# Optimization experiments

Hardware: AMD Instinct MI355X
Metric: run time of the kernel (lower is better)

## Reference

```python
import jax, jax.numpy as jnp
import numpy as np
from jax import lax

DIM = 512
HEADS = 8
SR = 2  # kernel_and_stride for the KV downsampling conv


def setup_inputs() -> dict:
    key = jax.random.key(0)
    k0, k1, k2, k3 = jax.random.split(key, 4)
    B, C, H, W = 4, DIM, 64, 64
    x = jax.random.normal(k0, (B, C, H, W), dtype=jnp.float32)
    # Conv weights in OIHW layout (matching torch)
    wq = jax.random.normal(k1, (C, C, 1, 1), dtype=jnp.float32) / np.sqrt(C)
    wkv = jax.random.normal(k2, (2 * C, C, SR, SR), dtype=jnp.float32) / np.sqrt(C * SR * SR)
    wout = jax.random.normal(k3, (C, C, 1, 1), dtype=jnp.float32) / np.sqrt(C)
    return {"x": x, "wq": wq, "wkv": wkv, "wout": wout}


def _attend(x, wq, wkv, wout):
    B, C, H, W = x.shape
    d = C // HEADS
    scale = d ** -0.5
    # to_q: 1x1 conv == channel matmul
    q = jnp.einsum('bchw,oc->bohw', x, wq[:, :, 0, 0])
    # to_kv: strided conv, downsamples spatial grid by SR
    kv = lax.conv_general_dilated(
        x, wkv, window_strides=(SR, SR), padding='VALID',
        dimension_numbers=('NCHW', 'OIHW', 'NCHW'))
    k, v = jnp.split(kv, 2, axis=1)  # each [B, C, H/SR, W/SR]

    def to_bhl(t):  # [B, (h d), X, Y] -> [B, h, X*Y, d]
        b, c, xh, xw = t.shape
        return t.reshape(b, HEADS, d, xh * xw).transpose(0, 1, 3, 2)

    qh, kh, vh = to_bhl(q), to_bhl(k), to_bhl(v)
    sim = jnp.einsum('bhid,bhjd->bhij', qh, kh) * scale
    attn = jax.nn.softmax(sim, axis=-1)
    out = jnp.einsum('bhij,bhjd->bhid', attn, vh)  # [B, h, HW, d]
    out = out.transpose(0, 1, 3, 2).reshape(B, C, H, W)
    return jnp.einsum('bchw,oc->bohw', out, wout[:, :, 0, 0])


def reference(x, wq, wkv, wout):
    return _attend(x, wq, wkv, wout)
```

## Files before the change

kernel.cpp:

```cpp
#include <hip/hip_runtime.h>
#include <hip/hip_bf16.h>

typedef __bf16 bf16x8 __attribute__((ext_vector_type(8)));
typedef float f32x4 __attribute__((ext_vector_type(4)));
typedef unsigned short ushort_t;
typedef ushort_t ushort8 __attribute__((ext_vector_type(8)));
typedef unsigned uint2v __attribute__((ext_vector_type(2)));
typedef unsigned uint4v __attribute__((ext_vector_type(4)));

#define DIM 512
#define HEADS 8
#define HD 64
#define HWN 4096
#define KVN 1024
#define KKV 2048
#define LOG2E 1.44269504f

__device__ __forceinline__ ushort_t f2bf(float f) {
    union { float f; unsigned u; } v; v.f = f;
    unsigned r = v.u + 0x7fffu + ((v.u >> 16) & 1u);
    return (ushort_t)(r >> 16);
}

__device__ __forceinline__ unsigned cvtpk(float lo, float hi) {
    unsigned r;
    asm("v_cvt_pk_bf16_f32 %0, %1, %2" : "=v"(r) : "v"(lo), "v"(hi));
    return r;
}

__device__ __forceinline__ void pl32swap(unsigned &a, unsigned &b) {
    asm("v_permlane32_swap_b32 %0, %1" : "+v"(a), "+v"(b));
}
__device__ __forceinline__ void pl16swap(unsigned &a, unsigned &b) {
    asm("v_permlane16_swap_b32 %0, %1" : "+v"(a), "+v"(b));
}

__device__ __forceinline__ bf16x8 frag4(unsigned a, unsigned b, unsigned c, unsigned d) {
    uint4v t; t[0] = a; t[1] = b; t[2] = c; t[3] = d;
    return __builtin_bit_cast(bf16x8, t);
}

__device__ __forceinline__ void gload_lds16(const ushort_t* g, ushort_t* l) {
    __builtin_amdgcn_global_load_lds(
        (const __attribute__((address_space(1))) unsigned int*)(const void*)g,
        (__attribute__((address_space(3))) unsigned int*)(void*)l,
        16, 0, 0);
}

__device__ __forceinline__ void kstep_mfma(
        const ushort_t* __restrict__ ldsA, const ushort_t* __restrict__ ldsB,
        int wm, int wn, int l15, int quad, f32x4 (&acc)[4][4]) {
    bf16x8 a[4], bb[4];
    #pragma unroll
    for (int i = 0; i < 4; ++i)
        a[i] = *(const bf16x8*)&ldsA[(wm + i * 16 + l15) * 32 + quad * 8];
    #pragma unroll
    for (int j = 0; j < 4; ++j)
        bb[j] = *(const bf16x8*)&ldsB[(wn + j * 16 + l15) * 32 + quad * 8];
    #pragma unroll
    for (int i = 0; i < 4; ++i)
        #pragma unroll
        for (int j = 0; j < 4; ++j)
            acc[i][j] = __builtin_amdgcn_mfma_f32_16x16x32_bf16(a[i], bb[j], acc[i][j], 0, 0, 0);
}

__global__ __launch_bounds__(256) void cvt_kernel(
        const float* __restrict__ src, ushort_t* __restrict__ dst, int n8) {
    int i = blockIdx.x * 256 + threadIdx.x;
    if (i >= n8) return;
    const float* p = &src[(size_t)i * 8];
    f32x4 v0 = *(const f32x4*)&p[0];
    f32x4 v1 = *(const f32x4*)&p[4];
    ushort8 w;
    w[0] = f2bf(v0[0]); w[1] = f2bf(v0[1]); w[2] = f2bf(v0[2]); w[3] = f2bf(v0[3]);
    w[4] = f2bf(v1[0]); w[5] = f2bf(v1[1]); w[6] = f2bf(v1[2]); w[7] = f2bf(v1[3]);
    *(ushort8*)&dst[i * 8] = w;
}

__global__ __launch_bounds__(256) void cvt_xT_kernel(
        const float* __restrict__ x, ushort_t* __restrict__ xT) {
    const int b  = blockIdx.z;
    const int c0 = blockIdx.y * 64;
    const int p0 = blockIdx.x * 64;
    __shared__ ushort_t tile[64 * 72];

    const int tid = threadIdx.x;
    {
        int r = tid >> 2, pc = (tid & 3) * 16;
        const float* src = &x[((size_t)b * DIM + c0 + r) * HWN + p0 + pc];
        f32x4 v0 = *(const f32x4*)&src[0];
        f32x4 v1 = *(const f32x4*)&src[4];
        f32x4 v2 = *(const f32x4*)&src[8];
        f32x4 v3 = *(const f32x4*)&src[12];
        ushort8 w0, w1;
        w0[0]=f2bf(v0[0]); w0[1]=f2bf(v0[1]); w0[2]=f2bf(v0[2]); w0[3]=f2bf(v0[3]);
        w0[4]=f2bf(v1[0]); w0[5]=f2bf(v1[1]); w0[6]=f2bf(v1[2]); w0[7]=f2bf(v1[3]);
        w1[0]=f2bf(v2[0]); w1[1]=f2bf(v2[1]); w1[2]=f2bf(v2[2]); w1[3]=f2bf(v2[3]);
        w1[4]=f2bf(v3[0]); w1[5]=f2bf(v3[1]); w1[6]=f2bf(v3[2]); w1[7]=f2bf(v3[3]);
        *(ushort8*)&tile[r * 72 + pc]     = w0;
        *(ushort8*)&tile[r * 72 + pc + 8] = w1;
    }
    __syncthreads();
    {
        int p = tid >> 2, cc = (tid & 3) * 16;
        ushort8 w0, w1;
        #pragma unroll
        for (int j = 0; j < 8; ++j) {
            w0[j] = tile[(cc + j) * 72 + p];
            w1[j] = tile[(cc + 8 + j) * 72 + p];
        }
        ushort_t* dst = &xT[((size_t)b * HWN + p0 + p) * DIM + c0 + cc];
        *(ushort8*)&dst[0] = w0;
        *(ushort8*)&dst[8] = w1;
    }
}

__global__ __launch_bounds__(256) void cvt_wkvT_kernel(
        const float* __restrict__ wkv, ushort_t* __restrict__ wkvT) {
    int i = blockIdx.x * 256 + threadIdx.x;
    if (i >= 1024 * 512) return;
    int o2 = i >> 9, c = i & 511;
    f32x4 v = *(const f32x4*)&wkv[(size_t)i * 4];
    #pragma unroll
    for (int q = 0; q < 4; ++q)
        wkvT[(size_t)o2 * KKV + q * 512 + c] = f2bf(v[q]);
}

__global__ __launch_bounds__(256) void qproj_kernel(
        const ushort_t* __restrict__ xT, const ushort_t* __restrict__ wqb,
        ushort_t* __restrict__ qs) {
    const int b  = blockIdx.z;
    const int m0 = blockIdx.y * 128;
    const int n0 = blockIdx.x * 128;

    __shared__ ushort_t ldsA[128 * 32];
    __shared__ ushort_t ldsB[128 * 32];

    const int tid  = threadIdx.x;
    const int wave = tid >> 6;
    const int lane = tid & 63;
    const int l15  = lane & 15;
    const int quad = lane >> 4;
    const int wm   = (wave >> 1) * 64;
    const int wn   = (wave & 1) * 64;

    const int srow = wave * 32 + (lane >> 2);
    const int schk = (lane & 3) * 8;
    const ushort_t* asrc = &wqb[(m0 + srow) * DIM + schk];
    const ushort_t* bsrc = &xT[((size_t)b * HWN + n0 + srow) * DIM + schk];
    ushort_t* adst = &ldsA[wave * 1024];
    ushort_t* bdst = &ldsB[wave * 1024];

    f32x4 zero = {0.f, 0.f, 0.f, 0.f};
    f32x4 acc[4][4];
    #pragma unroll
    for (int i = 0; i < 4; ++i)
        #pragma unroll
        for (int j = 0; j < 4; ++j) acc[i][j] = zero;

    for (int k0 = 0; k0 < DIM; k0 += 32) {
        gload_lds16(asrc + k0,            adst);
        gload_lds16(asrc + 16 * DIM + k0, adst + 512);
        gload_lds16(bsrc + k0,            bdst);
        gload_lds16(bsrc + 16 * DIM + k0, bdst + 512);
        __syncthreads();
        kstep_mfma(ldsA, ldsB, wm, wn, l15, quad, acc);
        __syncthreads();
    }

    #pragma unroll
    for (int i = 0; i < 4; ++i)
        #pragma unroll
        for (int j = 0; j < 4; ++j)
            #pragma unroll
            for (int r = 0; r < 4; ++r) {
                int m = m0 + wm + i * 16 + quad * 4 + r;
                int n = n0 + wn + j * 16 + l15;
                qs[((size_t)b * DIM + m) * HWN + n] =
                    f2bf(acc[i][j][r] * (0.125f * LOG2E));
            }
}

__global__ __launch_bounds__(256) void kv_kernel(
        const ushort_t* __restrict__ xT, const ushort_t* __restrict__ wkvT,
        ushort_t* __restrict__ ks, ushort_t* __restrict__ vt) {
    const int b  = blockIdx.z;
    const int m0 = blockIdx.y * 128;
    const int j0 = blockIdx.x * 128;

    __shared__ ushort_t sh[128 * 72];
    ushort_t* ldsA = sh;
    ushort_t* ldsB = sh + 4096;

    const int tid  = threadIdx.x;
    const int wave = tid >> 6;
    const int lane = tid & 63;
    const int l15  = lane & 15;
    const int quad = lane >> 4;
    const int wm   = (wave >> 1) * 64;
    const int wn   = (wave & 1) * 64;

    const int srow = wave * 32 + (lane >> 2);
    const int schk = (lane & 3) * 8;
    const int jr0 = j0 + srow, jr1 = jr0 + 16;
    const int y0 = jr0 >> 5, x0 = jr0 & 31;
    const int y1 = jr1 >> 5, x1 = jr1 & 31;

    const ushort_t* asrc = &wkvT[(size_t)(m0 + srow) * KKV + schk];
    ushort_t* adst = &ldsA[wave * 1024];
    ushort_t* bdst = &ldsB[wave * 1024];

    f32x4 zero = {0.f, 0.f, 0.f, 0.f};
    f32x4 acc[4][4];
    #pragma unroll
    for (int i = 0; i < 4; ++i)
        #pragma unroll
        for (int j = 0; j < 4; ++j) acc[i][j] = zero;

    for (int q = 0; q < 4; ++q) {
        const int di = q >> 1, dj = q & 1;
        const ushort_t* b0 =
            &xT[((size_t)b * HWN + (2 * y0 + di) * 64 + 2 * x0 + dj) * DIM + schk];
        const ushort_t* b1 =
            &xT[((size_t)b * HWN + (2 * y1 + di) * 64 + 2 * x1 + dj) * DIM + schk];
        const ushort_t* aq = asrc + q * 512;
        for (int kc = 0; kc < 512; kc += 32) {
            gload_lds16(aq + kc,                    adst);
            gload_lds16(aq + 16 * KKV + kc,         adst + 512);
            gload_lds16(b0 + kc,                    bdst);
            gload_lds16(b1 + kc,                    bdst + 512);
            __syncthreads();
            kstep_mfma(ldsA, ldsB, wm, wn, l15, quad, acc);
            __syncthreads();
        }
    }

    if (m0 < DIM) {
        const int h0 = m0 >> 6;
        #pragma unroll
        for (int mh = 0; mh < 2; ++mh) {
            if ((wave >> 1) == mh) {
                #pragma unroll
                for (int i = 0; i < 4; ++i)
                    #pragma unroll
                    for (int j = 0; j < 4; ++j)
                        #pragma unroll
                        for (int r = 0; r < 4; ++r) {
                            int mloc = i * 16 + quad * 4 + r;
                            int n    = wn + j * 16 + l15;
                            sh[n * 72 + mloc] = f2bf(acc[i][j][r]);
                        }
            }
            __syncthreads();
            {
                int n = tid >> 1, doff = (tid & 1) * 32;
                ushort8 u0 = *(const ushort8*)&sh[n * 72 + doff];
                ushort8 u1 = *(const ushort8*)&sh[n * 72 + doff + 8];
                ushort8 u2 = *(const ushort8*)&sh[n * 72 + doff + 16];
                ushort8 u3 = *(const ushort8*)&sh[n * 72 + doff + 24];
                ushort_t* dst =
                    &ks[(((size_t)b * HEADS + h0 + mh) * KVN + j0 + n) * HD + doff];
                *(ushort8*)&dst[0]  = u0;
                *(ushort8*)&dst[8]  = u1;
                *(ushort8*)&dst[16] = u2;
                *(ushort8*)&dst[24] = u3;
            }
            __syncthreads();
        }
    } else {
        #pragma unroll
        for (int i = 0; i < 4; ++i)
            #pragma unroll
            for (int j = 0; j < 4; ++j)
                #pragma unroll
                for (int r = 0; r < 4; ++r) {
                    int mfull = m0 - DIM + wm + i * 16 + quad * 4 + r;
                    int h  = mfull >> 6, dd = mfull & 63;
                    int n  = wn + j * 16 + l15;
                    vt[(((size_t)b * HEADS + h) * HD + dd) * KVN + j0 + n] =
                        f2bf(acc[i][j][r]);
                }
    }
}

__global__ __launch_bounds__(256, 2) void attn_kernel(
        const ushort_t* __restrict__ qs,
        const ushort_t* __restrict__ ks,
        const ushort_t* __restrict__ vt,
        ushort_t* __restrict__ ao) {
    const int b = blockIdx.z, h = blockIdx.y;
    const int tid = threadIdx.x, wave = tid >> 6, lane = tid & 63;
    const int l15 = lane & 15, quad = lane >> 4;
    const int s7  = l15 & 7;
    const int iw = blockIdx.x * 256 + wave * 64;

    __shared__ ushort_t ldsK[2][64 * 64];
    __shared__ ushort_t ldsV[2][64 * 64];

    const ushort_t* Kh = &ks[((size_t)b * HEADS + h) * (KVN * HD)];
    const ushort_t* Vh = &vt[((size_t)b * HEADS + h) * (HD * KVN)];

    const int srow = wave * 8 + (lane >> 3);
    const int schk = (lane & 7) ^ (lane >> 3);
    const ushort_t* kp0 = Kh + srow * HD + schk * 8;
    const ushort_t* kp1 = Kh + (srow + 32) * HD + schk * 8;
    const ushort_t* vp0 = Vh + (size_t)srow * KVN + schk * 8;
    const ushort_t* vp1 = Vh + (size_t)(srow + 32) * KVN + schk * 8;

    bf16x8 bq[4][2];
    #pragma unroll
    for (int ih = 0; ih < 4; ++ih)
        #pragma unroll
        for (int kk = 0; kk < 2; ++kk) {
            ushort8 t;
            #pragma unroll
            for (int j = 0; j < 8; ++j) {
                int c = h * HD + kk * 32 + quad * 8 + j;
                int p = iw + ih * 16 + l15;
                t[j] = qs[((size_t)b * DIM + c) * HWN + p];
            }
            bq[ih][kk] = *(bf16x8*)&t;
        }

    f32x4 zero = {0.f, 0.f, 0.f, 0.f};
    f32x4 o[4][4];
    #pragma unroll
    for (int ih = 0; ih < 4; ++ih)
        #pragma unroll
        for (int nt = 0; nt < 4; ++nt) o[ih][nt] = zero;
    float ssum[4] = {0.f, 0.f, 0.f, 0.f};

    gload_lds16(kp0, &ldsK[0][wave * 512]);
    gload_lds16(kp1, &ldsK[0][wave * 512 + 2048]);
    gload_lds16(vp0, &ldsV[0][wave * 512]);
    gload_lds16(vp1, &ldsV[0][wave * 512 + 2048]);
    asm volatile("s_waitcnt vmcnt(0)" ::: "memory");
    __syncthreads();

    for (int t = 0; t < 16; ++t) {
        const int cur = t & 1;
        if (t < 15) {
            const int jn = (t + 1) * 64;
            gload_lds16(kp0 + jn * HD, &ldsK[cur ^ 1][wave * 512]);
            gload_lds16(kp1 + jn * HD, &ldsK[cur ^ 1][wave * 512 + 2048]);
            gload_lds16(vp0 + jn,      &ldsV[cur ^ 1][wave * 512]);
            gload_lds16(vp1 + jn,      &ldsV[cur ^ 1][wave * 512 + 2048]);
        }

        unsigned P2[4][4][2];
        #pragma unroll
        for (int nt = 0; nt < 4; ++nt) {
            const ushort_t* kb = &ldsK[cur][(nt * 16 + l15) * 64];
            bf16x8 bk0 = *(const bf16x8*)&kb[(quad ^ s7) * 8];
            bf16x8 bk1 = *(const bf16x8*)&kb[((quad + 4) ^ s7) * 8];
            #pragma unroll
            for (int ih = 0; ih < 4; ++ih) {
                f32x4 s = zero;
                s = __builtin_amdgcn_mfma_f32_16x16x32_bf16(bk0, bq[ih][0], s, 0, 0, 0);
                s = __builtin_amdgcn_mfma_f32_16x16x32_bf16(bk1, bq[ih][1], s, 0, 0, 0);
                float p0 = __builtin_amdgcn_exp2f(s[0]);
                float p1 = __builtin_amdgcn_exp2f(s[1]);
                float p2 = __builtin_amdgcn_exp2f(s[2]);
                float p3 = __builtin_amdgcn_exp2f(s[3]);
                ssum[ih] += (p0 + p1) + (p2 + p3);
                P2[ih][nt][0] = cvtpk(p0, p1);
                P2[ih][nt][1] = cvtpk(p2, p3);
            }
        }

        #pragma unroll
        for (int ih = 0; ih < 4; ++ih)
            #pragma unroll
            for (int bh = 0; bh < 2; ++bh)
                #pragma unroll
                for (int rp = 0; rp < 2; ++rp) {
                    pl32swap(P2[ih][bh * 2][rp], P2[ih][bh * 2 + 1][rp]);
                    pl16swap(P2[ih][bh * 2][rp], P2[ih][bh * 2 + 1][rp]);
                }
        bf16x8 bp[4][2];
        #pragma unroll
        for (int ih = 0; ih < 4; ++ih) {
            bp[ih][0] = frag4(P2[ih][0][0], P2[ih][0][1], P2[ih][1][0], P2[ih][1][1]);
            bp[ih][1] = frag4(P2[ih][2][0], P2[ih][2][1], P2[ih][3][0], P2[ih][3][1]);
        }

        #pragma unroll
        for (int nt = 0; nt < 4; ++nt) {
            const ushort_t* vb = &ldsV[cur][(nt * 16 + l15) * 64];
            bf16x8 bv0 = *(const bf16x8*)&vb[(quad ^ s7) * 8];
            bf16x8 bv1 = *(const bf16x8*)&vb[((quad + 4) ^ s7) * 8];
            #pragma unroll
            for (int ih = 0; ih < 4; ++ih) {
                o[ih][nt] = __builtin_amdgcn_mfma_f32_16x16x32_bf16(bv0, bp[ih][0], o[ih][nt], 0, 0, 0);
                o[ih][nt] = __builtin_amdgcn_mfma_f32_16x16x32_bf16(bv1, bp[ih][1], o[ih][nt], 0, 0, 0);
            }
        }

        asm volatile("s_waitcnt vmcnt(0)" ::: "memory");
        __syncthreads();
    }

    #pragma unroll
    for (int ih = 0; ih < 4; ++ih) {
        float tsum = ssum[ih];
        tsum += __shfl_xor(tsum, 16);
        tsum += __shfl_xor(tsum, 32);
        float invl = 1.0f / tsum;
        int i = iw + ih * 16 + l15;
        ushort_t* dst = &ao[((size_t)b * HWN + i) * DIM + h * HD];
        #pragma unroll
        for (int nt = 0; nt < 4; ++nt) {
            unsigned d0 = cvtpk(o[ih][nt][0] * invl, o[ih][nt][1] * invl);
            unsigned d1 = cvtpk(o[ih][nt][2] * invl, o[ih][nt][3] * invl);
            uint2v w; w[0] = d0; w[1] = d1;
            *(uint2v*)&dst[nt * 16 + quad * 4] = w;
        }
    }
}

__global__ __launch_bounds__(256) void outproj_kernel(
        const ushort_t* __restrict__ ao, const ushort_t* __restrict__ woutb,
        float* __restrict__ out) {
    const int b  = blockIdx.z;
    const int m0 = blockIdx.y * 128;
    const int n0 = blockIdx.x * 128;

    __shared__ ushort_t ldsA[128 * 32];
    __shared__ ushort_t ldsB[128 * 32];

    const int tid  = threadIdx.x;
    const int wave = tid >> 6;
    const int lane = tid & 63;
    const int l15  = lane & 15;
    const int quad = lane >> 4;
    const int wm   = (wave >> 1) * 64;
    const int wn   = (wave & 1) * 64;

    const int srow = wave * 32 + (lane >> 2);
    const int schk = (lane & 3) * 8;
    const ushort_t* asrc = &woutb[(m0 + srow) * DIM + schk];
    const ushort_t* bsrc = &ao[((size_t)b * HWN + n0 + srow) * DIM + schk];
    ushort_t* adst = &ldsA[wave * 1024];
    ushort_t* bdst = &ldsB[wave * 1024];

    f32x4 zero = {0.f, 0.f, 0.f, 0.f};
    f32x4 acc[4][4];
    #pragma unroll
    for (int i = 0; i < 4; ++i)
        #pragma unroll
        for (int j = 0; j < 4; ++j) acc[i][j] = zero;

    for (int k0 = 0; k0 < DIM; k0 += 32) {
        gload_lds16(asrc + k0,            adst);
        gload_lds16(asrc + 16 * DIM + k0, adst + 512);
        gload_lds16(bsrc + k0,            bdst);
        gload_lds16(bsrc + 16 * DIM + k0, bdst + 512);
        __syncthreads();
        kstep_mfma(ldsA, ldsB, wm, wn, l15, quad, acc);
        __syncthreads();
    }

    #pragma unroll
    for (int i = 0; i < 4; ++i)
        #pragma unroll
        for (int j = 0; j < 4; ++j)
            #pragma unroll
            for (int r = 0; r < 4; ++r) {
                int m = m0 + wm + i * 16 + quad * 4 + r;
                int n = n0 + wn + j * 16 + l15;
                out[((size_t)b * DIM + m) * HWN + n] = acc[i][j][r];
            }
}

extern "C" void kernel_launch(void* const* d_in, const int* in_sizes, int n_in,
                              void* d_out, int out_size, void* d_ws, size_t ws_size,
                              hipStream_t stream) {
    const float* x    = (const float*)d_in[0];
    const float* wq   = (const float*)d_in[1];
    const float* wkv  = (const float*)d_in[2];
    const float* wout = (const float*)d_in[3];
    float* out = (float*)d_out;

    char* ws = (char*)d_ws;
    ushort_t* xT    = (ushort_t*)(ws);
    ushort_t* qsb   = (ushort_t*)(ws + 16777216);
    ushort_t* ksb   = (ushort_t*)(ws + 33554432);
    ushort_t* vtb   = (ushort_t*)(ws + 37748736);
    ushort_t* aob   = (ushort_t*)(ws + 41943040);
    ushort_t* wqb   = (ushort_t*)(ws + 58720256);
    ushort_t* wkvT  = (ushort_t*)(ws + 59244544);
    ushort_t* woutb = (ushort_t*)(ws + 63438848);

    cvt_xT_kernel  <<<dim3(64, 8, 4), 256, 0, stream>>>(x, xT);
    cvt_kernel     <<<dim3(128),      256, 0, stream>>>(wq, wqb, 32768);
    cvt_wkvT_kernel<<<dim3(2048),     256, 0, stream>>>(wkv, wkvT);
    cvt_kernel     <<<dim3(128),      256, 0, stream>>>(wout, woutb, 32768);

    qproj_kernel  <<<dim3(32, 4, 4),  256, 0, stream>>>(xT, wqb, qsb);
    kv_kernel     <<<dim3(8, 8, 4),   256, 0, stream>>>(xT, wkvT, ksb, vtb);
    attn_kernel   <<<dim3(16, 8, 4),  256, 0, stream>>>(qsb, ksb, vtb, aob);
    outproj_kernel<<<dim3(32, 4, 4),  256, 0, stream>>>(aob, woutb, out);
}
```

Baseline: 218.0 us.

## Double-buffer LDS with BK=64 in projection GEMM kernels

The q-projection, kv-projection and output-projection GEMMs now use a K tile of 64 instead of 32, with two LDS buffers per operand. Global-to-LDS loads for the next tile are issued before the MFMAs on the current tile. This halves the number of barriers per K and hides global load latency behind compute. In exchange LDS use grows to 64KB per block, which may lower occupancy, and the row stride of 64 bf16 may cause LDS bank conflicts on the fragment reads.

```diff
diff --git a/kernel.cpp b/kernel.cpp
--- a/kernel.cpp
+++ b/kernel.cpp
@@ -47,21 +47,9 @@
         16, 0, 0);
 }
 
-__device__ __forceinline__ void kstep_mfma(
-        const ushort_t* __restrict__ ldsA, const ushort_t* __restrict__ ldsB,
-        int wm, int wn, int l15, int quad, f32x4 (&acc)[4][4]) {
-    bf16x8 a[4], bb[4];
-    #pragma unroll
-    for (int i = 0; i < 4; ++i)
-        a[i] = *(const bf16x8*)&ldsA[(wm + i * 16 + l15) * 32 + quad * 8];
-    #pragma unroll
-    for (int j = 0; j < 4; ++j)
-        bb[j] = *(const bf16x8*)&ldsB[(wn + j * 16 + l15) * 32 + quad * 8];
-    #pragma unroll
-    for (int i = 0; i < 4; ++i)
-        #pragma unroll
-        for (int j = 0; j < 4; ++j)
-            acc[i][j] = __builtin_amdgcn_mfma_f32_16x16x32_bf16(a[i], bb[j], acc[i][j], 0, 0, 0);
+__device__ __forceinline__ void drain_sync() {
+    asm volatile("s_waitcnt vmcnt(0)" ::: "memory");
+    __syncthreads();
 }
 
 __global__ __launch_bounds__(256) void cvt_kernel(
@@ -126,6 +114,26 @@
         wkvT[(size_t)o2 * KKV + q * 512 + c] = f2bf(v[q]);
 }
 
+__device__ __forceinline__ void gemm_compute64(
+        const ushort_t* __restrict__ sA, const ushort_t* __restrict__ sB,
+        int wm, int wn, int l15, int quad, f32x4 (&acc)[4][4]) {
+    bf16x8 a[2][4], bb[2][4];
+    #pragma unroll
+    for (int kk = 0; kk < 2; ++kk)
+        #pragma unroll
+        for (int i = 0; i < 4; ++i) {
+            a[kk][i]  = *(const bf16x8*)&sA[(wm + i * 16 + l15) * 64 + (kk * 4 + quad) * 8];
+            bb[kk][i] = *(const bf16x8*)&sB[(wn + i * 16 + l15) * 64 + (kk * 4 + quad) * 8];
+        }
+    #pragma unroll
+    for (int i = 0; i < 4; ++i)
+        #pragma unroll
+        for (int j = 0; j < 4; ++j) {
+            acc[i][j] = __builtin_amdgcn_mfma_f32_16x16x32_bf16(a[0][i], bb[0][j], acc[i][j], 0, 0, 0);
+            acc[i][j] = __builtin_amdgcn_mfma_f32_16x16x32_bf16(a[1][i], bb[1][j], acc[i][j], 0, 0, 0);
+        }
+}
+
 __global__ __launch_bounds__(256) void qproj_kernel(
         const ushort_t* __restrict__ xT, const ushort_t* __restrict__ wqb,
         ushort_t* __restrict__ qs) {
@@ -133,8 +141,8 @@
     const int m0 = blockIdx.y * 128;
     const int n0 = blockIdx.x * 128;
 
-    __shared__ ushort_t ldsA[128 * 32];
-    __shared__ ushort_t ldsB[128 * 32];
+    __shared__ ushort_t shA[2][128 * 64];
+    __shared__ ushort_t shB[2][128 * 64];
 
     const int tid  = threadIdx.x;
     const int wave = tid >> 6;
@@ -143,13 +151,18 @@
     const int quad = lane >> 4;
     const int wm   = (wave >> 1) * 64;
     const int wn   = (wave & 1) * 64;
-
-    const int srow = wave * 32 + (lane >> 2);
-    const int schk = (lane & 3) * 8;
-    const ushort_t* asrc = &wqb[(m0 + srow) * DIM + schk];
-    const ushort_t* bsrc = &xT[((size_t)b * HWN + n0 + srow) * DIM + schk];
-    ushort_t* adst = &ldsA[wave * 1024];
-    ushort_t* bdst = &ldsB[wave * 1024];
+    const int r8   = lane >> 3;
+    const int c8   = lane & 7;
+
+    const ushort_t* aS[4];
+    const ushort_t* bS[4];
+    #pragma unroll
+    for (int g = 0; g < 4; ++g) {
+        int row = wave * 32 + g * 8 + r8;
+        aS[g] = &wqb[(size_t)(m0 + row) * DIM + c8 * 8];
+        bS[g] = &xT[((size_t)b * HWN + n0 + row) * DIM + c8 * 8];
+    }
+    const int ldso = wave * 32 * 64;
 
     f32x4 zero = {0.f, 0.f, 0.f, 0.f};
     f32x4 acc[4][4];
@@ -158,14 +171,25 @@
         #pragma unroll
         for (int j = 0; j < 4; ++j) acc[i][j] = zero;
 
-    for (int k0 = 0; k0 < DIM; k0 += 32) {
-        gload_lds16(asrc + k0,            adst);
-        gload_lds16(asrc + 16 * DIM + k0, adst + 512);
-        gload_lds16(bsrc + k0,            bdst);
-        gload_lds16(bsrc + 16 * DIM + k0, bdst + 512);
-        __syncthreads();
-        kstep_mfma(ldsA, ldsB, wm, wn, l15, quad, acc);
-        __syncthreads();
+    #pragma unroll
+    for (int g = 0; g < 4; ++g) {
+        gload_lds16(aS[g], &shA[0][ldso + g * 512]);
+        gload_lds16(bS[g], &shB[0][ldso + g * 512]);
+    }
+    drain_sync();
+
+    for (int t = 0; t < 8; ++t) {
+        const int cur = t & 1;
+        if (t < 7) {
+            const int ko = (t + 1) * 64;
+            #pragma unroll
+            for (int g = 0; g < 4; ++g) {
+                gload_lds16(aS[g] + ko, &shA[cur ^ 1][ldso + g * 512]);
+                gload_lds16(bS[g] + ko, &shB[cur ^ 1][ldso + g * 512]);
+            }
+        }
+        gemm_compute64(shA[cur], shB[cur], wm, wn, l15, quad, acc);
+        drain_sync();
     }
 
     #pragma unroll
@@ -188,9 +212,8 @@
     const int m0 = blockIdx.y * 128;
     const int j0 = blockIdx.x * 128;
 
-    __shared__ ushort_t sh[128 * 72];
-    ushort_t* ldsA = sh;
-    ushort_t* ldsB = sh + 4096;
+    __shared__ ushort_t shA[2][128 * 64];
+    __shared__ ushort_t shB[2][128 * 64];
 
     const int tid  = threadIdx.x;
     const int wave = tid >> 6;
@@ -199,16 +222,20 @@
     const int quad = lane >> 4;
     const int wm   = (wave >> 1) * 64;
     const int wn   = (wave & 1) * 64;
-
-    const int srow = wave * 32 + (lane >> 2);
-    const int schk = (lane & 3) * 8;
-    const int jr0 = j0 + srow, jr1 = jr0 + 16;
-    const int y0 = jr0 >> 5, x0 = jr0 & 31;
-    const int y1 = jr1 >> 5, x1 = jr1 & 31;
-
-    const ushort_t* asrc = &wkvT[(size_t)(m0 + srow) * KKV + schk];
-    ushort_t* adst = &ldsA[wave * 1024];
-    ushort_t* bdst = &ldsB[wave * 1024];
+    const int r8   = lane >> 3;
+    const int c8   = lane & 7;
+
+    const ushort_t* aS[4];
+    const ushort_t* bS[4];
+    #pragma unroll
+    for (int g = 0; g < 4; ++g) {
+        int row = wave * 32 + g * 8 + r8;
+        aS[g] = &wkvT[(size_t)(m0 + row) * KKV + c8 * 8];
+        int jr = j0 + row;
+        int y = jr >> 5, x = jr & 31;
+        bS[g] = &xT[((size_t)b * HWN + 128 * y + 2 * x) * DIM + c8 * 8];
+    }
+    const int ldso = wave * 32 * 64;
 
     f32x4 zero = {0.f, 0.f, 0.f, 0.f};
     f32x4 acc[4][4];
@@ -217,25 +244,32 @@
         #pragma unroll
         for (int j = 0; j < 4; ++j) acc[i][j] = zero;
 
-    for (int q = 0; q < 4; ++q) {
-        const int di = q >> 1, dj = q & 1;
-        const ushort_t* b0 =
-            &xT[((size_t)b * HWN + (2 * y0 + di) * 64 + 2 * x0 + dj) * DIM + schk];
-        const ushort_t* b1 =
-            &xT[((size_t)b * HWN + (2 * y1 + di) * 64 + 2 * x1 + dj) * DIM + schk];
-        const ushort_t* aq = asrc + q * 512;
-        for (int kc = 0; kc < 512; kc += 32) {
-            gload_lds16(aq + kc,                    adst);
-            gload_lds16(aq + 16 * KKV + kc,         adst + 512);
-            gload_lds16(b0 + kc,                    bdst);
-            gload_lds16(b1 + kc,                    bdst + 512);
-            __syncthreads();
-            kstep_mfma(ldsA, ldsB, wm, wn, l15, quad, acc);
-            __syncthreads();
-        }
+    #pragma unroll
+    for (int g = 0; g < 4; ++g) {
+        gload_lds16(aS[g], &shA[0][ldso + g * 512]);
+        gload_lds16(bS[g], &shB[0][ldso + g * 512]);
+    }
+    drain_sync();
+
+    for (int t = 0; t < 32; ++t) {
+        const int cur = t & 1;
+        if (t < 31) {
+            const int tn = t + 1;
+            const int qn = tn >> 3;
+            const int ao = tn * 64;
+            const int bo = (64 * (qn >> 1) + (qn & 1)) * DIM + (tn & 7) * 64;
+            #pragma unroll
+            for (int g = 0; g < 4; ++g) {
+                gload_lds16(aS[g] + ao, &shA[cur ^ 1][ldso + g * 512]);
+                gload_lds16(bS[g] + bo, &shB[cur ^ 1][ldso + g * 512]);
+            }
+        }
+        gemm_compute64(shA[cur], shB[cur], wm, wn, l15, quad, acc);
+        drain_sync();
     }
 
     if (m0 < DIM) {
+        ushort_t* cbuf = &shA[0][0];
         const int h0 = m0 >> 6;
         #pragma unroll
         for (int mh = 0; mh < 2; ++mh) {
@@ -248,16 +282,16 @@
                         for (int r = 0; r < 4; ++r) {
                             int mloc = i * 16 + quad * 4 + r;
                             int n    = wn + j * 16 + l15;
-                            sh[n * 72 + mloc] = f2bf(acc[i][j][r]);
+                            cbuf[n * 72 + mloc] = f2bf(acc[i][j][r]);
                         }
             }
             __syncthreads();
             {
                 int n = tid >> 1, doff = (tid & 1) * 32;
-                ushort8 u0 = *(const ushort8*)&sh[n * 72 + doff];
-                ushort8 u1 = *(const ushort8*)&sh[n * 72 + doff + 8];
-                ushort8 u2 = *(const ushort8*)&sh[n * 72 + doff + 16];
-                ushort8 u3 = *(const ushort8*)&sh[n * 72 + doff + 24];
+                ushort8 u0 = *(const ushort8*)&cbuf[n * 72 + doff];
+                ushort8 u1 = *(const ushort8*)&cbuf[n * 72 + doff + 8];
+                ushort8 u2 = *(const ushort8*)&cbuf[n * 72 + doff + 16];
+                ushort8 u3 = *(const ushort8*)&cbuf[n * 72 + doff + 24];
                 ushort_t* dst =
                     &ks[(((size_t)b * HEADS + h0 + mh) * KVN + j0 + n) * HD + doff];
                 *(ushort8*)&dst[0]  = u0;
@@ -425,8 +459,8 @@
     const int m0 = blockIdx.y * 128;
     const int n0 = blockIdx.x * 128;
 
-    __shared__ ushort_t ldsA[128 * 32];
-    __shared__ ushort_t ldsB[128 * 32];
+    __shared__ ushort_t shA[2][128 * 64];
+    __shared__ ushort_t shB[2][128 * 64];
 
     const int tid  = threadIdx.x;
     const int wave = tid >> 6;
@@ -435,13 +469,18 @@
     const int quad = lane >> 4;
     const int wm   = (wave >> 1) * 64;
     const int wn   = (wave & 1) * 64;
-
-    const int srow = wave * 32 + (lane >> 2);
-    const int schk = (lane & 3) * 8;
-    const ushort_t* asrc = &woutb[(m0 + srow) * DIM + schk];
-    const ushort_t* bsrc = &ao[((size_t)b * HWN + n0 + srow) * DIM + schk];
-    ushort_t* adst = &ldsA[wave * 1024];
-    ushort_t* bdst = &ldsB[wave * 1024];
+    const int r8   = lane >> 3;
+    const int c8   = lane & 7;
+
+    const ushort_t* aS[4];
+    const ushort_t* bS[4];
+    #pragma unroll
+    for (int g = 0; g < 4; ++g) {
+        int row = wave * 32 + g * 8 + r8;
+        aS[g] = &woutb[(size_t)(m0 + row) * DIM + c8 * 8];
+        bS[g] = &ao[((size_t)b * HWN + n0 + row) * DIM + c8 * 8];
+    }
+    const int ldso = wave * 32 * 64;
 
     f32x4 zero = {0.f, 0.f, 0.f, 0.f};
     f32x4 acc[4][4];
@@ -450,14 +489,25 @@
         #pragma unroll
         for (int j = 0; j < 4; ++j) acc[i][j] = zero;
 
-    for (int k0 = 0; k0 < DIM; k0 += 32) {
-        gload_lds16(asrc + k0,            adst);
-        gload_lds16(asrc + 16 * DIM + k0, adst + 512);
-        gload_lds16(bsrc + k0,            bdst);
-        gload_lds16(bsrc + 16 * DIM + k0, bdst + 512);
-        __syncthreads();
-        kstep_mfma(ldsA, ldsB, wm, wn, l15, quad, acc);
-        __syncthreads();
+    #pragma unroll
+    for (int g = 0; g < 4; ++g) {
+        gload_lds16(aS[g], &shA[0][ldso + g * 512]);
+        gload_lds16(bS[g], &shB[0][ldso + g * 512]);
+    }
+    drain_sync();
+
+    for (int t = 0; t < 8; ++t) {
+        const int cur = t & 1;
+        if (t < 7) {
+            const int ko = (t + 1) * 64;
+            #pragma unroll
+            for (int g = 0; g < 4; ++g) {
+                gload_lds16(aS[g] + ko, &shA[cur ^ 1][ldso + g * 512]);
+                gload_lds16(bS[g] + ko, &shB[cur ^ 1][ldso + g * 512]);
+            }
+        }
+        gemm_compute64(shA[cur], shB[cur], wm, wn, l15, quad, acc);
+        drain_sync();
     }
 
     #pragma unroll
```

Measured after the change: 234.4 us. 7.5% more time.
